# Kernel tuning notes

Measured on AMD Instinct MI355X. Metric: run time of the kernel, lower is better.

Reference implementation:

```python
import jax, jax.numpy as jnp
import numpy as np
import math

EPS_PHI = 1e-4
EPS_DEN = 1e-6

B, H, N, D = 4, 16, 4096, 64
M = 128  # num random features


def _phi(x, omega, is_query):
    # x: [B,H,N,D], omega: [M,D] -> [B,H,N,M]
    proj = jnp.einsum('bhnd,md->bhnm', x, omega)
    log_phi = proj - 0.5 * jnp.sum(x * x, axis=-1, keepdims=True)
    if is_query:
        log_phi = log_phi - jnp.max(log_phi, axis=-1, keepdims=True)
    else:
        log_phi = log_phi - jnp.max(log_phi)
    return jnp.exp(log_phi) / math.sqrt(omega.shape[0]) + EPS_PHI


def setup_inputs() -> dict:
    key = jax.random.key(0)
    kq, kk, kv, ko = jax.random.split(key, 4)
    return {
        'q': jax.random.normal(kq, (B, H, N, D), dtype=jnp.float32),
        'k': jax.random.normal(kk, (B, H, N, D), dtype=jnp.float32),
        'v': jax.random.normal(kv, (B, H, N, D), dtype=jnp.float32),
        'omega': jax.random.normal(ko, (M, D), dtype=jnp.float32),
    }


def reference(q, k, v, omega):
    scale = q.shape[-1] ** (-0.25)
    phi_q = _phi(q * scale, omega, is_query=True).astype(jnp.float32)
    phi_k = _phi(k * scale, omega, is_query=False).astype(jnp.float32)
    vf = v.astype(jnp.float32)

    b, h, n, m = phi_q.shape
    d = vf.shape[-1]
    # time-major for scan: [N,B,H,*]
    pq_t = jnp.moveaxis(phi_q, 2, 0)
    pk_t = jnp.moveaxis(phi_k, 2, 0)
    v_t = jnp.moveaxis(vf, 2, 0)

    S0 = jnp.zeros((b, h, m, d), jnp.float32)
    z0 = jnp.zeros((b, h, m), jnp.float32)

    def step(carry, inp):
        S, z = carry
        pq_i, pk_i, v_i = inp  # [B,H,M], [B,H,M], [B,H,D]
        S = S + jnp.einsum('bhm,bhd->bhmd', pk_i, v_i)
        z = z + pk_i
        num = jnp.einsum('bhm,bhmd->bhd', pq_i, S)
        den = jnp.sum(pq_i * z, axis=-1, keepdims=True) + EPS_DEN
        return (S, z), num / den

    _, out_t = jax.lax.scan(step, (S0, z0), (pq_t, pk_t, v_t))
    out = jnp.moveaxis(out_t, 0, 2)  # [B,H,N,D]
    return out.astype(q.dtype)
```

## Files before the change

### kernel.cpp

```cpp
#include <hip/hip_runtime.h>
#include <math.h>

#define Bq 4
#define Hq 16
#define Nq 4096
#define Dq 64
#define Mq 128
#define Cq 32
#define Lq 128
#define EPS_PHI 1e-4f
#define EPS_DEN 1e-6f
#define SCALE 0.35355339059327373f
#define INVSQRT_M 0.08838834764831845f
#define STATE_STRIDE 8320

#define PSTR 264
#define KSTR 136
#define WSTR 264

#define PERM(m) (((m) & 15) * 8 + ((m) >> 4))

typedef __attribute__((ext_vector_type(8))) short bf16x8;
typedef __attribute__((ext_vector_type(4))) short s16x4;
typedef __attribute__((ext_vector_type(4))) float f32x4;

static __device__ inline f32x4 mfma16(bf16x8 a, bf16x8 b, f32x4 c) {
    return __builtin_amdgcn_mfma_f32_16x16x32_bf16(a, b, c, 0, 0, 0);
}

static __device__ inline unsigned short f2bf(float f) {
    unsigned u = __builtin_bit_cast(unsigned, f);
    u += 0x7FFF + ((u >> 16) & 1);
    return (unsigned short)(u >> 16);
}

static __device__ inline bf16x8 gfrag(const float* p, float scale) {
    float4 a = *(const float4*)p;
    float4 b = *(const float4*)(p + 4);
    union { bf16x8 v; unsigned short s[8]; } u;
    u.s[0] = f2bf(a.x * scale); u.s[1] = f2bf(a.y * scale);
    u.s[2] = f2bf(a.z * scale); u.s[3] = f2bf(a.w * scale);
    u.s[4] = f2bf(b.x * scale); u.s[5] = f2bf(b.y * scale);
    u.s[6] = f2bf(b.z * scale); u.s[7] = f2bf(b.w * scale);
    return u.v;
}

__global__ __launch_bounds__(512, 4) void chunkstate_kernel(
    const float* __restrict__ kin, const float* __restrict__ vin,
    const float* __restrict__ omega, float* __restrict__ rowK,
    float* __restrict__ partial, float* __restrict__ Sbuf,
    float* __restrict__ csumV) {
    __shared__ __align__(16) unsigned short PKt[128 * KSTR];
    __shared__ __align__(16) unsigned short Vt[80 * KSTR];
    __shared__ float h_lds[128];
    __shared__ float wred[8];
    __shared__ float csum[8][64];
    const int t = threadIdx.x, w = t >> 6, lane = t & 63;
    const int c16 = lane & 15, qd = lane >> 4;
    const int bx = blockIdx.x;
    const size_t rowbase = (size_t)(bx >> 5) * Nq + (size_t)(bx & 31) * Lq;
    const float* kb = kin + rowbase * 64;
    const float* vb = vin + rowbase * 64;

    #pragma unroll
    for (int rep = 0; rep < 16; ++rep) {
        int e = rep * 512 + t;
        int l = rep * 8 + w;
        float x = kb[e] * SCALE;
        float s = x * x;
        #pragma unroll
        for (int o = 1; o <= 32; o <<= 1) s += __shfl_xor(s, o);
        if (lane == 0) { h_lds[l] = 0.5f * s; rowK[rowbase + l] = 0.5f * s; }
    }
    __syncthreads();

    f32x4 acc[8];
    #pragma unroll
    for (int nt = 0; nt < 8; ++nt) acc[nt] = (f32x4){0.f, 0.f, 0.f, 0.f};
    #pragma unroll
    for (int kt = 0; kt < 2; ++kt) {
        bf16x8 a = gfrag(kb + (size_t)(16 * w + c16) * 64 + kt * 32 + qd * 8, SCALE);
        #pragma unroll
        for (int nt = 0; nt < 8; ++nt) {
            bf16x8 b = gfrag(omega + (size_t)(16 * nt + c16) * 64 + kt * 32 + qd * 8, 1.0f);
            acc[nt] = mfma16(a, b, acc[nt]);
        }
    }
    const int row0 = 16 * w + 4 * qd;
    float lmax = -1e30f;
    #pragma unroll
    for (int r = 0; r < 4; ++r) {
        float h = h_lds[row0 + r];
        #pragma unroll
        for (int nt = 0; nt < 8; ++nt) lmax = fmaxf(lmax, acc[nt][r] - h);
    }
    #pragma unroll
    for (int o = 1; o <= 32; o <<= 1) lmax = fmaxf(lmax, __shfl_xor(lmax, o));
    if (lane == 0) wred[w] = lmax;
    {
        const int d = t & 63, g = t >> 6;
        float s = 0.f;
        #pragma unroll
        for (int j = 0; j < 16; ++j) s += vb[(16 * g + j) * 64 + d];
        csum[g][d] = s;
    }
    __syncthreads();
    float mc = wred[0];
    #pragma unroll
    for (int i = 1; i < 8; ++i) mc = fmaxf(mc, wred[i]);
    if (t == 0) partial[bx] = mc;

    #pragma unroll
    for (int nt = 0; nt < 8; ++nt) {
        union { s16x4 v; unsigned short s[4]; } u;
        #pragma unroll
        for (int r = 0; r < 4; ++r) {
            float pk = __expf(acc[nt][r] - h_lds[row0 + r] - mc) * INVSQRT_M;
            u.s[r] = f2bf(pk);
        }
        *(s16x4*)&PKt[(16 * nt + c16) * KSTR + row0] = u.v;
    }
    #pragma unroll
    for (int rep = 0; rep < 8; ++rep) {
        int e2 = rep * 512 + t;
        int d = e2 & 63, l2 = e2 >> 6;
        unsigned a = f2bf(vb[(2 * l2) * 64 + d]);
        unsigned b = f2bf(vb[(2 * l2 + 1) * 64 + d]);
        *(unsigned*)&Vt[d * KSTR + 2 * l2] = a | (b << 16);
    }
    if (t < 128) Vt[64 * KSTR + t] = 0x3F80;
    __syncthreads();

    f32x4 acc2[5];
    #pragma unroll
    for (int nt = 0; nt < 5; ++nt) acc2[nt] = (f32x4){0.f, 0.f, 0.f, 0.f};
    #pragma unroll
    for (int kt = 0; kt < 4; ++kt) {
        bf16x8 a = *(const bf16x8*)&PKt[(16 * w + c16) * KSTR + kt * 32 + qd * 8];
        #pragma unroll
        for (int nt = 0; nt < 5; ++nt) {
            bf16x8 b = *(const bf16x8*)&Vt[(16 * nt + c16) * KSTR + kt * 32 + qd * 8];
            acc2[nt] = mfma16(a, b, acc2[nt]);
        }
    }
    float* sb = Sbuf + (size_t)bx * STATE_STRIDE;
    #pragma unroll
    for (int r = 0; r < 4; ++r) {
        #pragma unroll
        for (int nt = 0; nt < 4; ++nt)
            sb[(row0 + r) * 64 + 16 * nt + c16] = acc2[nt][r];
        if (c16 == 0) sb[8192 + row0 + r] = acc2[4][r];
    }
    if (t < 64) {
        float s = 0.f;
        #pragma unroll
        for (int g = 0; g < 8; ++g) s += csum[g][t];
        csumV[(size_t)bx * 64 + t] = s;
    }
}

__global__ void gmax_kernel(const float* __restrict__ partial, int n, float* __restrict__ gmax) {
    float m = -1e30f;
    for (int i = threadIdx.x; i < n; i += 256) m = fmaxf(m, partial[i]);
    #pragma unroll
    for (int o = 1; o <= 32; o <<= 1) m = fmaxf(m, __shfl_xor(m, o));
    __shared__ float w[4];
    if ((threadIdx.x & 63) == 0) w[threadIdx.x >> 6] = m;
    __syncthreads();
    if (threadIdx.x == 0) gmax[0] = fmaxf(fmaxf(w[0], w[1]), fmaxf(w[2], w[3]));
}

#define PBLK 33
__global__ __launch_bounds__(256) void prefix_kernel(
    float* __restrict__ Sbuf, const float* __restrict__ csumV,
    const float* __restrict__ partial, const float* __restrict__ gmaxp) {
    const int bh = blockIdx.x / PBLK;
    const int e = (blockIdx.x % PBLK) * 256 + threadIdx.x;
    if (e >= STATE_STRIDE) return;
    const float gm = gmaxp[0];
    const int isZ = (e >= 8192);
    const int d = e & 63;
    float running = 0.f;
    size_t idx = (size_t)bh * Cq * STATE_STRIDE + e;
    #pragma unroll 4
    for (int c = 0; c < Cq; ++c, idx += STATE_STRIDE) {
        const int cx = bh * Cq + c;
        float sc = __expf(partial[cx] - gm);
        float epsterm = isZ ? (EPS_PHI * 128.0f)
                            : (EPS_PHI * csumV[(size_t)cx * 64 + d]);
        float tmp = sc * Sbuf[idx] + epsterm;
        Sbuf[idx] = running;
        running += tmp;
    }
}

__global__ __launch_bounds__(512, 2) void replay_kernel(
    const float* __restrict__ q, const float* __restrict__ kin,
    const float* __restrict__ vin, const float* __restrict__ omega,
    const float* __restrict__ rowK, const float* __restrict__ gmaxp,
    const float* __restrict__ Sbuf, float* __restrict__ out) {
    __shared__ __align__(16) unsigned short P[128 * PSTR];
    __shared__ __align__(16) unsigned short PK[128 * KSTR];
    __shared__ __align__(16) unsigned short Wt[65 * WSTR];
    const int t = threadIdx.x, w = t >> 6, lane = t & 63;
    const int c16 = lane & 15, qd = lane >> 4;
    const int bx = blockIdx.x;
    const size_t rowbase = (size_t)(bx >> 5) * Nq + (size_t)(bx & 31) * Lq;
    const float* qb = q + rowbase * 64;
    const float* kb = kin + rowbase * 64;
    const float* vb = vin + rowbase * 64;
    const float gmax = gmaxp[0];
    const int row0 = 16 * w + 4 * qd;
    const int arow = 16 * w + c16;

    f32x4 accq[8], acck[8];
    #pragma unroll
    for (int nt = 0; nt < 8; ++nt) {
        accq[nt] = (f32x4){0.f, 0.f, 0.f, 0.f};
        acck[nt] = (f32x4){0.f, 0.f, 0.f, 0.f};
    }
    #pragma unroll
    for (int kt = 0; kt < 2; ++kt) {
        bf16x8 aq = gfrag(qb + (size_t)arow * 64 + kt * 32 + qd * 8, SCALE);
        bf16x8 ak = gfrag(kb + (size_t)arow * 64 + kt * 32 + qd * 8, SCALE);
        #pragma unroll
        for (int nt = 0; nt < 8; ++nt) {
            bf16x8 b = gfrag(omega + (size_t)(16 * nt + c16) * 64 + kt * 32 + qd * 8, 1.0f);
            accq[nt] = mfma16(aq, b, accq[nt]);
            acck[nt] = mfma16(ak, b, acck[nt]);
        }
    }
    #pragma unroll
    for (int r = 0; r < 4; ++r) {
        float mx = accq[0][r];
        #pragma unroll
        for (int nt = 1; nt < 8; ++nt) mx = fmaxf(mx, accq[nt][r]);
        mx = fmaxf(mx, __shfl_xor(mx, 1));
        mx = fmaxf(mx, __shfl_xor(mx, 2));
        mx = fmaxf(mx, __shfl_xor(mx, 4));
        mx = fmaxf(mx, __shfl_xor(mx, 8));
        union { bf16x8 v; unsigned short s[8]; } u;
        #pragma unroll
        for (int nt = 0; nt < 8; ++nt)
            u.s[nt] = f2bf(__expf(accq[nt][r] - mx) * INVSQRT_M + EPS_PHI);
        *(bf16x8*)&P[(row0 + r) * PSTR + 128 + c16 * 8] = u.v;
    }
    #pragma unroll
    for (int r = 0; r < 4; ++r) {
        float h = rowK[rowbase + row0 + r];
        union { bf16x8 v; unsigned short s[8]; } u;
        #pragma unroll
        for (int nt = 0; nt < 8; ++nt)
            u.s[nt] = f2bf(__expf(acck[nt][r] - h - gmax) * INVSQRT_M + EPS_PHI);
        *(bf16x8*)&PK[(row0 + r) * KSTR + c16 * 8] = u.v;
    }
    const float* sb = Sbuf + (size_t)bx * STATE_STRIDE;
    #pragma unroll
    for (int rep = 0; rep < 8; ++rep) {
        int e2 = rep * 512 + t;
        int d = e2 & 63, l2 = e2 >> 6;
        unsigned a = f2bf(vb[(2 * l2) * 64 + d]);
        unsigned b = f2bf(vb[(2 * l2 + 1) * 64 + d]);
        *(unsigned*)&Wt[d * WSTR + 2 * l2] = a | (b << 16);
    }
    #pragma unroll
    for (int rep = 0; rep < 16; ++rep) {
        int e = rep * 512 + t;
        int m = e >> 6, d = e & 63;
        Wt[d * WSTR + 128 + PERM(m)] = f2bf(sb[e]);
    }
    if (t < 128)      Wt[64 * WSTR + t] = 0x3F80;
    else if (t < 256) Wt[64 * WSTR + 128 + PERM(t - 128)] = f2bf(sb[8192 + (t - 128)]);
    __syncthreads();

    bf16x8 bq[4];
    #pragma unroll
    for (int kt = 0; kt < 4; ++kt)
        bq[kt] = *(const bf16x8*)&P[arow * PSTR + 128 + kt * 32 + qd * 8];
    #pragma unroll
    for (int lt = 0; lt < 8; ++lt) {
        f32x4 a1 = (f32x4){0.f, 0.f, 0.f, 0.f};
        #pragma unroll
        for (int kt = 0; kt < 4; ++kt) {
            bf16x8 a = *(const bf16x8*)&PK[(16 * lt + c16) * KSTR + kt * 32 + qd * 8];
            a1 = mfma16(a, bq[kt], a1);
        }
        union { s16x4 v; unsigned short s[4]; } u;
        #pragma unroll
        for (int r = 0; r < 4; ++r) {
            int l = 16 * lt + 4 * qd + r;
            u.s[r] = f2bf((l <= arow) ? a1[r] : 0.f);
        }
        *(s16x4*)&P[arow * PSTR + 16 * lt + 4 * qd] = u.v;
    }
    f32x4 acc2[5];
    #pragma unroll
    for (int nt = 0; nt < 5; ++nt) acc2[nt] = (f32x4){0.f, 0.f, 0.f, 0.f};
    #pragma unroll
    for (int kt = 0; kt < 8; ++kt) {
        bf16x8 a = *(const bf16x8*)&P[arow * PSTR + kt * 32 + qd * 8];
        #pragma unroll
        for (int nt = 0; nt < 5; ++nt) {
            bf16x8 b = *(const bf16x8*)&Wt[(16 * nt + c16) * WSTR + kt * 32 + qd * 8];
            acc2[nt] = mfma16(a, b, acc2[nt]);
        }
    }
    #pragma unroll
    for (int r = 0; r < 4; ++r) {
        float den = __shfl(acc2[4][r], lane & 48) + EPS_DEN;
        float rd = 1.0f / den;
        #pragma unroll
        for (int nt = 0; nt < 4; ++nt)
            out[(rowbase + row0 + r) * 64 + 16 * nt + c16] = acc2[nt][r] * rd;
    }
}

extern "C" void kernel_launch(void* const* d_in, const int* in_sizes, int n_in,
                              void* d_out, int out_size, void* d_ws, size_t ws_size,
                              hipStream_t stream) {
    const float* q     = (const float*)d_in[0];
    const float* k     = (const float*)d_in[1];
    const float* v     = (const float*)d_in[2];
    const float* omega = (const float*)d_in[3];
    float* out = (float*)d_out;
    float* ws  = (float*)d_ws;

    const int totalRows = Bq * Hq * Nq;
    const int nChunks   = Bq * Hq * Cq;
    float* rowK    = ws;
    float* partial = rowK + totalRows;
    float* gmax    = partial + nChunks;
    float* Sbuf    = gmax + 16;
    float* csumV   = Sbuf + (size_t)nChunks * STATE_STRIDE;

    chunkstate_kernel<<<nChunks, 512, 0, stream>>>(k, v, omega, rowK, partial, Sbuf, csumV);
    gmax_kernel<<<1, 256, 0, stream>>>(partial, nChunks, gmax);
    prefix_kernel<<<64 * PBLK, 256, 0, stream>>>(Sbuf, csumV, partial, gmax);
    replay_kernel<<<nChunks, 512, 0, stream>>>(q, k, v, omega, rowK, gmax, Sbuf, out);
}
```

Before: 436.8 us.

## Keep replay intermediates in registers via shuffles, fuse row-norm into fragment loads

```diff
diff --git a/kernel.cpp b/kernel.cpp
--- a/kernel.cpp
+++ b/kernel.cpp
@@ -14,7 +14,6 @@
 #define INVSQRT_M 0.08838834764831845f
 #define STATE_STRIDE 8320
 
-#define PSTR 264
 #define KSTR 136
 #define WSTR 264
 
@@ -45,14 +44,26 @@
     return u.v;
 }
 
+static __device__ inline bf16x8 gfrag_h(const float* p, float* hs) {
+    float4 a = *(const float4*)p;
+    float4 b = *(const float4*)(p + 4);
+    float x0 = a.x * SCALE, x1 = a.y * SCALE, x2 = a.z * SCALE, x3 = a.w * SCALE;
+    float x4 = b.x * SCALE, x5 = b.y * SCALE, x6 = b.z * SCALE, x7 = b.w * SCALE;
+    *hs += x0 * x0 + x1 * x1 + x2 * x2 + x3 * x3
+         + x4 * x4 + x5 * x5 + x6 * x6 + x7 * x7;
+    union { bf16x8 v; unsigned short s[8]; } u;
+    u.s[0] = f2bf(x0); u.s[1] = f2bf(x1); u.s[2] = f2bf(x2); u.s[3] = f2bf(x3);
+    u.s[4] = f2bf(x4); u.s[5] = f2bf(x5); u.s[6] = f2bf(x6); u.s[7] = f2bf(x7);
+    return u.v;
+}
+
 __global__ __launch_bounds__(512, 4) void chunkstate_kernel(
     const float* __restrict__ kin, const float* __restrict__ vin,
-    const float* __restrict__ omega, float* __restrict__ rowK,
+    const float* __restrict__ omega,
     float* __restrict__ partial, float* __restrict__ Sbuf,
     float* __restrict__ csumV) {
     __shared__ __align__(16) unsigned short PKt[128 * KSTR];
     __shared__ __align__(16) unsigned short Vt[80 * KSTR];
-    __shared__ float h_lds[128];
     __shared__ float wred[8];
     __shared__ float csum[8][64];
     const int t = threadIdx.x, w = t >> 6, lane = t & 63;
@@ -62,37 +73,32 @@
     const float* kb = kin + rowbase * 64;
     const float* vb = vin + rowbase * 64;
 
-    #pragma unroll
-    for (int rep = 0; rep < 16; ++rep) {
-        int e = rep * 512 + t;
-        int l = rep * 8 + w;
-        float x = kb[e] * SCALE;
-        float s = x * x;
-        #pragma unroll
-        for (int o = 1; o <= 32; o <<= 1) s += __shfl_xor(s, o);
-        if (lane == 0) { h_lds[l] = 0.5f * s; rowK[rowbase + l] = 0.5f * s; }
-    }
-    __syncthreads();
-
     f32x4 acc[8];
+    float ssum = 0.f;
     #pragma unroll
     for (int nt = 0; nt < 8; ++nt) acc[nt] = (f32x4){0.f, 0.f, 0.f, 0.f};
     #pragma unroll
     for (int kt = 0; kt < 2; ++kt) {
-        bf16x8 a = gfrag(kb + (size_t)(16 * w + c16) * 64 + kt * 32 + qd * 8, SCALE);
+        bf16x8 a = gfrag_h(kb + (size_t)(16 * w + c16) * 64 + kt * 32 + qd * 8, &ssum);
         #pragma unroll
         for (int nt = 0; nt < 8; ++nt) {
             bf16x8 b = gfrag(omega + (size_t)(16 * nt + c16) * 64 + kt * 32 + qd * 8, 1.0f);
             acc[nt] = mfma16(a, b, acc[nt]);
         }
     }
+    ssum += __shfl_xor(ssum, 16);
+    ssum += __shfl_xor(ssum, 32);
+    const float h_red = 0.5f * ssum;
     const int row0 = 16 * w + 4 * qd;
+    float h4[4];
+    #pragma unroll
+    for (int r = 0; r < 4; ++r) h4[r] = __shfl(h_red, 4 * qd + r);
+
     float lmax = -1e30f;
     #pragma unroll
     for (int r = 0; r < 4; ++r) {
-        float h = h_lds[row0 + r];
-        #pragma unroll
-        for (int nt = 0; nt < 8; ++nt) lmax = fmaxf(lmax, acc[nt][r] - h);
+        #pragma unroll
+        for (int nt = 0; nt < 8; ++nt) lmax = fmaxf(lmax, acc[nt][r] - h4[r]);
     }
     #pragma unroll
     for (int o = 1; o <= 32; o <<= 1) lmax = fmaxf(lmax, __shfl_xor(lmax, o));
@@ -103,22 +109,6 @@
         #pragma unroll
         for (int j = 0; j < 16; ++j) s += vb[(16 * g + j) * 64 + d];
         csum[g][d] = s;
-    }
-    __syncthreads();
-    float mc = wred[0];
-    #pragma unroll
-    for (int i = 1; i < 8; ++i) mc = fmaxf(mc, wred[i]);
-    if (t == 0) partial[bx] = mc;
-
-    #pragma unroll
-    for (int nt = 0; nt < 8; ++nt) {
-        union { s16x4 v; unsigned short s[4]; } u;
-        #pragma unroll
-        for (int r = 0; r < 4; ++r) {
-            float pk = __expf(acc[nt][r] - h_lds[row0 + r] - mc) * INVSQRT_M;
-            u.s[r] = f2bf(pk);
-        }
-        *(s16x4*)&PKt[(16 * nt + c16) * KSTR + row0] = u.v;
     }
     #pragma unroll
     for (int rep = 0; rep < 8; ++rep) {
@@ -129,6 +119,22 @@
         *(unsigned*)&Vt[d * KSTR + 2 * l2] = a | (b << 16);
     }
     if (t < 128) Vt[64 * KSTR + t] = 0x3F80;
+    __syncthreads();
+    float mc = wred[0];
+    #pragma unroll
+    for (int i = 1; i < 8; ++i) mc = fmaxf(mc, wred[i]);
+    if (t == 0) partial[bx] = mc;
+
+    #pragma unroll
+    for (int nt = 0; nt < 8; ++nt) {
+        union { s16x4 v; unsigned short s[4]; } u;
+        #pragma unroll
+        for (int r = 0; r < 4; ++r) {
+            float pk = __expf(acc[nt][r] - h4[r] - mc) * INVSQRT_M;
+            u.s[r] = f2bf(pk);
+        }
+        *(s16x4*)&PKt[(16 * nt + c16) * KSTR + row0] = u.v;
+    }
     __syncthreads();
 
     f32x4 acc2[5];
@@ -180,28 +186,31 @@
     const float gm = gmaxp[0];
     const int isZ = (e >= 8192);
     const int d = e & 63;
+    const size_t base = (size_t)bh * Cq * STATE_STRIDE + e;
+
+    float vals[Cq];
+    #pragma unroll
+    for (int c = 0; c < Cq; ++c) vals[c] = Sbuf[base + (size_t)c * STATE_STRIDE];
+
     float running = 0.f;
-    size_t idx = (size_t)bh * Cq * STATE_STRIDE + e;
-    #pragma unroll 4
-    for (int c = 0; c < Cq; ++c, idx += STATE_STRIDE) {
+    #pragma unroll
+    for (int c = 0; c < Cq; ++c) {
         const int cx = bh * Cq + c;
         float sc = __expf(partial[cx] - gm);
-        float epsterm = isZ ? (EPS_PHI * 128.0f)
-                            : (EPS_PHI * csumV[(size_t)cx * 64 + d]);
-        float tmp = sc * Sbuf[idx] + epsterm;
-        Sbuf[idx] = running;
-        running += tmp;
-    }
-}
-
-__global__ __launch_bounds__(512, 2) void replay_kernel(
+        float ep = isZ ? (EPS_PHI * 128.0f) : (EPS_PHI * csumV[(size_t)cx * 64 + d]);
+        float v = sc * vals[c] + ep;
+        Sbuf[base + (size_t)c * STATE_STRIDE] = running;
+        running += v;
+    }
+}
+
+__global__ __launch_bounds__(512, 4) void replay_kernel(
     const float* __restrict__ q, const float* __restrict__ kin,
     const float* __restrict__ vin, const float* __restrict__ omega,
-    const float* __restrict__ rowK, const float* __restrict__ gmaxp,
-    const float* __restrict__ Sbuf, float* __restrict__ out) {
-    __shared__ __align__(16) unsigned short P[128 * PSTR];
+    const float* __restrict__ gmaxp, const float* __restrict__ Sbuf,
+    float* __restrict__ out) {
     __shared__ __align__(16) unsigned short PK[128 * KSTR];
-    __shared__ __align__(16) unsigned short Wt[65 * WSTR];
+    __shared__ __align__(16) unsigned short Wt[80 * WSTR];
     const int t = threadIdx.x, w = t >> 6, lane = t & 63;
     const int c16 = lane & 15, qd = lane >> 4;
     const int bx = blockIdx.x;
@@ -214,6 +223,7 @@
     const int arow = 16 * w + c16;
 
     f32x4 accq[8], acck[8];
+    float ssum = 0.f;
     #pragma unroll
     for (int nt = 0; nt < 8; ++nt) {
         accq[nt] = (f32x4){0.f, 0.f, 0.f, 0.f};
@@ -222,7 +232,7 @@
     #pragma unroll
     for (int kt = 0; kt < 2; ++kt) {
         bf16x8 aq = gfrag(qb + (size_t)arow * 64 + kt * 32 + qd * 8, SCALE);
-        bf16x8 ak = gfrag(kb + (size_t)arow * 64 + kt * 32 + qd * 8, SCALE);
+        bf16x8 ak = gfrag_h(kb + (size_t)arow * 64 + kt * 32 + qd * 8, &ssum);
         #pragma unroll
         for (int nt = 0; nt < 8; ++nt) {
             bf16x8 b = gfrag(omega + (size_t)(16 * nt + c16) * 64 + kt * 32 + qd * 8, 1.0f);
@@ -230,6 +240,11 @@
             acck[nt] = mfma16(ak, b, acck[nt]);
         }
     }
+    ssum += __shfl_xor(ssum, 16);
+    ssum += __shfl_xor(ssum, 32);
+    const float h_red = 0.5f * ssum;
+
+    unsigned pqu[4][4];
     #pragma unroll
     for (int r = 0; r < 4; ++r) {
         float mx = accq[0][r];
@@ -239,15 +254,36 @@
         mx = fmaxf(mx, __shfl_xor(mx, 2));
         mx = fmaxf(mx, __shfl_xor(mx, 4));
         mx = fmaxf(mx, __shfl_xor(mx, 8));
-        union { bf16x8 v; unsigned short s[8]; } u;
-        #pragma unroll
-        for (int nt = 0; nt < 8; ++nt)
-            u.s[nt] = f2bf(__expf(accq[nt][r] - mx) * INVSQRT_M + EPS_PHI);
-        *(bf16x8*)&P[(row0 + r) * PSTR + 128 + c16 * 8] = u.v;
-    }
-    #pragma unroll
-    for (int r = 0; r < 4; ++r) {
-        float h = rowK[rowbase + row0 + r];
+        #pragma unroll
+        for (int i = 0; i < 4; ++i) {
+            float lo = __expf(accq[2 * i][r]     - mx) * INVSQRT_M + EPS_PHI;
+            float hi = __expf(accq[2 * i + 1][r] - mx) * INVSQRT_M + EPS_PHI;
+            pqu[r][i] = (unsigned)f2bf(lo) | ((unsigned)f2bf(hi) << 16);
+        }
+    }
+    bf16x8 bq[4];
+    {
+        const int rsel = c16 & 3;
+        #pragma unroll
+        for (int kt = 0; kt < 4; ++kt) {
+            const int src = 4 * kt + qd + ((c16 >> 2) << 4);
+            union { bf16x8 v; unsigned u[4]; } tt;
+            #pragma unroll
+            for (int i = 0; i < 4; ++i) {
+                unsigned v0 = __shfl(pqu[0][i], src);
+                unsigned v1 = __shfl(pqu[1][i], src);
+                unsigned v2 = __shfl(pqu[2][i], src);
+                unsigned v3 = __shfl(pqu[3][i], src);
+                unsigned s01 = (rsel & 1) ? v1 : v0;
+                unsigned s23 = (rsel & 1) ? v3 : v2;
+                tt.u[i] = (rsel & 2) ? s23 : s01;
+            }
+            bq[kt] = tt.v;
+        }
+    }
+    #pragma unroll
+    for (int r = 0; r < 4; ++r) {
+        float h = __shfl(h_red, 4 * qd + r);
         union { bf16x8 v; unsigned short s[8]; } u;
         #pragma unroll
         for (int nt = 0; nt < 8; ++nt)
@@ -273,36 +309,58 @@
     else if (t < 256) Wt[64 * WSTR + 128 + PERM(t - 128)] = f2bf(sb[8192 + (t - 128)]);
     __syncthreads();
 
-    bf16x8 bq[4];
-    #pragma unroll
-    for (int kt = 0; kt < 4; ++kt)
-        bq[kt] = *(const bf16x8*)&P[arow * PSTR + 128 + kt * 32 + qd * 8];
+    f32x4 a1[8];
     #pragma unroll
     for (int lt = 0; lt < 8; ++lt) {
-        f32x4 a1 = (f32x4){0.f, 0.f, 0.f, 0.f};
+        a1[lt] = (f32x4){0.f, 0.f, 0.f, 0.f};
         #pragma unroll
         for (int kt = 0; kt < 4; ++kt) {
             bf16x8 a = *(const bf16x8*)&PK[(16 * lt + c16) * KSTR + kt * 32 + qd * 8];
-            a1 = mfma16(a, bq[kt], a1);
-        }
-        union { s16x4 v; unsigned short s[4]; } u;
-        #pragma unroll
-        for (int r = 0; r < 4; ++r) {
-            int l = 16 * lt + 4 * qd + r;
-            u.s[r] = f2bf((l <= arow) ? a1[r] : 0.f);
-        }
-        *(s16x4*)&P[arow * PSTR + 16 * lt + 4 * qd] = u.v;
+            a1[lt] = mfma16(a, bq[kt], a1[lt]);
+        }
+    }
+    unsigned asu[8][2];
+    #pragma unroll
+    for (int lt = 0; lt < 8; ++lt) {
+        const int lbase = 16 * lt + 4 * qd;
+        float m0 = (lbase + 0 <= arow) ? a1[lt][0] : 0.f;
+        float m1 = (lbase + 1 <= arow) ? a1[lt][1] : 0.f;
+        float m2 = (lbase + 2 <= arow) ? a1[lt][2] : 0.f;
+        float m3 = (lbase + 3 <= arow) ? a1[lt][3] : 0.f;
+        asu[lt][0] = (unsigned)f2bf(m0) | ((unsigned)f2bf(m1) << 16);
+        asu[lt][1] = (unsigned)f2bf(m2) | ((unsigned)f2bf(m3) << 16);
     }
     f32x4 acc2[5];
     #pragma unroll
     for (int nt = 0; nt < 5; ++nt) acc2[nt] = (f32x4){0.f, 0.f, 0.f, 0.f};
-    #pragma unroll
-    for (int kt = 0; kt < 8; ++kt) {
-        bf16x8 a = *(const bf16x8*)&P[arow * PSTR + kt * 32 + qd * 8];
-        #pragma unroll
-        for (int nt = 0; nt < 5; ++nt) {
-            bf16x8 b = *(const bf16x8*)&Wt[(16 * nt + c16) * WSTR + kt * 32 + qd * 8];
-            acc2[nt] = mfma16(a, b, acc2[nt]);
+    {
+        const int src0 = c16 + ((2 * qd) & 3) * 16;
+        const int src1 = c16 + ((2 * qd + 1) & 3) * 16;
+        const int hsel = qd >> 1;
+        #pragma unroll
+        for (int kt = 0; kt < 4; ++kt) {
+            union { bf16x8 v; unsigned u[4]; } af;
+            unsigned a00 = __shfl(asu[2 * kt][0], src0), a10 = __shfl(asu[2 * kt + 1][0], src0);
+            unsigned a01 = __shfl(asu[2 * kt][1], src0), a11 = __shfl(asu[2 * kt + 1][1], src0);
+            af.u[0] = hsel ? a10 : a00;
+            af.u[1] = hsel ? a11 : a01;
+            unsigned b00 = __shfl(asu[2 * kt][0], src1), b10 = __shfl(asu[2 * kt + 1][0], src1);
+            unsigned b01 = __shfl(asu[2 * kt][1], src1), b11 = __shfl(asu[2 * kt + 1][1], src1);
+            af.u[2] = hsel ? b10 : b00;
+            af.u[3] = hsel ? b11 : b01;
+            #pragma unroll
+            for (int nt = 0; nt < 5; ++nt) {
+                bf16x8 b = *(const bf16x8*)&Wt[(16 * nt + c16) * WSTR + kt * 32 + qd * 8];
+                acc2[nt] = mfma16(af.v, b, acc2[nt]);
+            }
+        }
+        #pragma unroll
+        for (int kt = 4; kt < 8; ++kt) {
+            #pragma unroll
+            for (int nt = 0; nt < 5; ++nt) {
+                bf16x8 b = *(const bf16x8*)&Wt[(16 * nt + c16) * WSTR + kt * 32 + qd * 8];
+                acc2[nt] = mfma16(bq[kt - 4], b, acc2[nt]);
+            }
         }
     }
     #pragma unroll
@@ -325,16 +383,14 @@
     float* out = (float*)d_out;
     float* ws  = (float*)d_ws;
 
-    const int totalRows = Bq * Hq * Nq;
-    const int nChunks   = Bq * Hq * Cq;
-    float* rowK    = ws;
-    float* partial = rowK + totalRows;
+    const int nChunks = Bq * Hq * Cq;
+    float* partial = ws;
     float* gmax    = partial + nChunks;
     float* Sbuf    = gmax + 16;
     float* csumV   = Sbuf + (size_t)nChunks * STATE_STRIDE;
 
-    chunkstate_kernel<<<nChunks, 512, 0, stream>>>(k, v, omega, rowK, partial, Sbuf, csumV);
+    chunkstate_kernel<<<nChunks, 512, 0, stream>>>(k, v, omega, partial, Sbuf, csumV);
     gmax_kernel<<<1, 256, 0, stream>>>(partial, nChunks, gmax);
     prefix_kernel<<<64 * PBLK, 256, 0, stream>>>(Sbuf, csumV, partial, gmax);
-    replay_kernel<<<nChunks, 512, 0, stream>>>(q, k, v, omega, rowK, gmax, Sbuf, out);
-}
+    replay_kernel<<<nChunks, 512, 0, stream>>>(q, k, v, omega, gmax, Sbuf, out);
+}
```

New measurement: 360.8 us. 1.21x faster.
